# Kernel tuning notes

Measured on AMD Instinct MI355X. Metric: run time of the kernel, lower is better.

## Reference

```python
import jax, jax.numpy as jnp
import numpy as np

N_NODES = 8192
D = 384
N_EDGES = 262144
N_REL = 4
N_LAYERS = 2
BATCH = 64


def setup_inputs() -> dict:
    key = jax.random.key(0)
    ks = jax.random.split(key, 8)
    x = jax.random.normal(ks[0], (N_NODES, D), jnp.float32)
    edge_index = jax.random.randint(ks[1], (2, N_EDGES), 0, N_NODES, dtype=jnp.int32)
    edge_type = jax.random.randint(ks[2], (N_EDGES,), 0, N_REL, dtype=jnp.int32)
    s = 1.0 / np.sqrt(D)
    W_rel = jax.random.uniform(ks[3], (N_LAYERS, N_REL, D, D), jnp.float32, -s, s)
    b_rel = jnp.zeros((N_LAYERS, N_REL, D), jnp.float32)
    norm_const = jnp.ones((N_LAYERS, N_REL), jnp.float32)
    W_msg = jax.random.uniform(ks[4], (N_LAYERS, D, D), jnp.float32, -s, s)
    b_msg = jnp.zeros((N_LAYERS, D), jnp.float32)
    W_self = jax.random.uniform(ks[5], (N_LAYERS, D, D), jnp.float32, -s, s)
    b_self = jnp.zeros((N_LAYERS, D), jnp.float32)
    bn_gamma = jnp.ones((D,), jnp.float32)
    bn_beta = jnp.zeros((D,), jnp.float32)
    return {"x": x, "edge_index": edge_index, "edge_type": edge_type,
            "bn_gamma": bn_gamma, "bn_beta": bn_beta,
            "W_rel": W_rel, "b_rel": b_rel, "norm_const": norm_const,
            "W_msg": W_msg, "b_msg": b_msg, "W_self": W_self, "b_self": b_self,
            "batch_size": BATCH}


def _seg_sum(v, idx, n):
    return jax.ops.segment_sum(v, idx, num_segments=n)


def _forward(x, bn_gamma, bn_beta, W_rel, b_rel, norm_const, W_msg, b_msg,
             W_self, b_self, edge_index, edge_type, batch_size):
    n = x.shape[0]
    # BatchNorm1d (training-mode batch stats) on the utterance embeddings
    mu = x.mean(axis=0)
    var = x.var(axis=0)
    h = bn_gamma * (x - mu) * jax.lax.rsqrt(var + 1e-5) + bn_beta
    src, dst = edge_index[0], edge_index[1]  # PyG: row=source(j), col=target(i)
    # pairwise cosine similarity, gathered only at the edges actually used:
    # edge_weights[dst, src] = <h_dst, h_src> / (|h_dst||h_src|)
    xn = h / jnp.linalg.norm(h, axis=1, keepdims=True)
    w_e = jnp.sum(xn[dst] * xn[src], axis=-1)  # [E]
    ones_e = jnp.ones(src.shape[0], jnp.float32)
    n_layers, n_rel = W_rel.shape[0], W_rel.shape[1]
    for l in range(n_layers):
        # RelationAwareMP: per-relation linear + weighted scatter-mean, summed
        out = jnp.zeros((n, W_rel.shape[2]), h.dtype)
        for r in range(n_rel):
            mask = (edge_type == r).astype(h.dtype)  # [E]
            xr = h @ W_rel[l, r].T + b_rel[l, r]  # [N, D]
            coef = mask * w_e / norm_const[l, r]  # [E]
            s = _seg_sum(coef[:, None] * xr[src], dst, n)
            c = _seg_sum(mask, dst, n)
            out = out + s / jnp.maximum(c, 1.0)[:, None]
        rel_out = jax.nn.relu(out)
        # MP: relu(mean_j lin(x_j) + self_lin(x)), then residual
        mj = rel_out @ W_msg[l].T + b_msg[l]
        s = _seg_sum(mj[src], dst, n)
        c = _seg_sum(ones_e, dst, n)
        aggr = s / jnp.maximum(c, 1.0)[:, None]
        h = jax.nn.relu(aggr + rel_out @ W_self[l].T + b_self[l]) + h
    return h.reshape(batch_size, -1, h.shape[-1]).mean(axis=1)


def reference(x, edge_index, edge_type, bn_gamma, bn_beta, W_rel, b_rel,
              norm_const, W_msg, b_msg, W_self, b_self, batch_size):
    return _forward(x, bn_gamma, bn_beta, W_rel, b_rel, norm_const,
                    W_msg, b_msg, W_self, b_self,
                    edge_index, edge_type, batch_size)
```

## Files before the change

kernel.cpp:

```cpp
#include <hip/hip_runtime.h>
#include <hip/hip_bf16.h>

#define NN 8192
#define DD 384
#define NE 262144
#define NR 4
#define NL 2
#define NB 64

typedef __attribute__((ext_vector_type(8))) short bf16x8;
typedef __attribute__((ext_vector_type(4))) float f32x4;

__device__ __forceinline__ unsigned short f2bf(float f) {
  unsigned u = __float_as_uint(f);
  unsigned r = (u + 0x7fffu + ((u >> 16) & 1u)) >> 16;
  return (unsigned short)r;
}
__device__ __forceinline__ unsigned pack_bf2(float lo, float hi) {
  return (unsigned)f2bf(lo) | ((unsigned)f2bf(hi) << 16);
}
__device__ __forceinline__ float bflo(unsigned u) { return __uint_as_float(u << 16); }
__device__ __forceinline__ float bfhi(unsigned u) { return __uint_as_float(u & 0xffff0000u); }
__device__ __forceinline__ void gl_lds16(const void* g, void* l) {
  __builtin_amdgcn_global_load_lds(
      (const __attribute__((address_space(1))) unsigned int*)g,
      (__attribute__((address_space(3))) unsigned int*)l, 16, 0, 0);
}
__device__ __forceinline__ float dot8(uint4 a, uint4 b) {
  return bflo(a.x) * bflo(b.x) + bfhi(a.x) * bfhi(b.x) +
         bflo(a.y) * bflo(b.y) + bfhi(a.y) * bfhi(b.y) +
         bflo(a.z) * bflo(b.z) + bfhi(a.z) * bfhi(b.z) +
         bflo(a.w) * bflo(b.w) + bfhi(a.w) * bfhi(b.w);
}

__global__ void k_zero(uint4* __restrict__ p, int n4) {
  int i = blockIdx.x * 256 + threadIdx.x;
  if (i < n4) p[i] = make_uint4(0, 0, 0, 0);
}

__global__ void k_colstats(const float* __restrict__ x, float* __restrict__ musum,
                           float* __restrict__ msqsum) {
  int c = threadIdx.x;
  int r0 = blockIdx.x * 32;
  float s = 0.f, s2 = 0.f;
  for (int r = 0; r < 32; ++r) {
    float v = x[(size_t)(r0 + r) * DD + c];
    s += v; s2 += v * v;
  }
  atomicAdd(&musum[c], s);
  atomicAdd(&msqsum[c], s2);
}

__global__ void k_bn(const float* __restrict__ x, const float* __restrict__ gamma,
                     const float* __restrict__ beta, const float* __restrict__ musum,
                     const float* __restrict__ msqsum, float* __restrict__ h,
                     short* __restrict__ h_bf, float* __restrict__ ninv) {
  int n = blockIdx.x;
  int t = threadIdx.x;
  float ss = 0.f;
#pragma unroll
  for (int i = 0; i < 6; ++i) {
    int c = t + i * 64;
    float m = musum[c] * (1.f / NN);
    float var = msqsum[c] * (1.f / NN) - m * m;
    float v = gamma[c] * (x[(size_t)n * DD + c] - m) * rsqrtf(var + 1e-5f) + beta[c];
    h[(size_t)n * DD + c] = v;
    h_bf[(size_t)n * DD + c] = (short)f2bf(v);
    ss += v * v;
  }
#pragma unroll
  for (int m = 32; m; m >>= 1) ss += __shfl_xor(ss, m, 64);
  if (t == 0) ninv[n] = rsqrtf(ss);
}

__global__ void k_counts(const int* __restrict__ ei, const int* __restrict__ et,
                         int* __restrict__ c_rel) {
  int e = blockIdx.x * blockDim.x + threadIdx.x;
  if (e >= NE) return;
  int dst = ei[NE + e];
  atomicAdd(&c_rel[dst * NR + et[e]], 1);
}

__global__ void k_scan(const int* __restrict__ c_rel, int* __restrict__ rp2,
                       int* __restrict__ cursor) {
  __shared__ int part[1024];
  int t = threadIdx.x;
  int base = t * 32;
  int v[32]; int s = 0;
#pragma unroll
  for (int i = 0; i < 32; ++i) { v[i] = c_rel[base + i]; s += v[i]; }
  part[t] = s;
  __syncthreads();
  for (int off = 1; off < 1024; off <<= 1) {
    int add = (t >= off) ? part[t - off] : 0;
    __syncthreads();
    part[t] += add;
    __syncthreads();
  }
  int run = (t == 0) ? 0 : part[t - 1];
  if (t == 0) rp2[0] = 0;
#pragma unroll
  for (int i = 0; i < 32; ++i) {
    cursor[base + i] = run;
    run += v[i];
    rp2[base + i + 1] = run;
  }
}

__global__ void k_fill(const int* __restrict__ ei, const int* __restrict__ et,
                       int* __restrict__ cursor, int* __restrict__ meta) {
  int e = blockIdx.x * blockDim.x + threadIdx.x;
  if (e >= NE) return;
  int src = ei[e], dst = ei[NE + e];
  int pos = atomicAdd(&cursor[dst * NR + et[e]], 1);
  meta[pos] = src;
}

__global__ void k_we2(const short* __restrict__ hb, const float* __restrict__ ninv,
                      const int* __restrict__ rp2, const int* __restrict__ meta,
                      float* __restrict__ wsort) {
  int n = blockIdx.x;
  int g = threadIdx.x >> 4, sl = threadIdx.x & 15;
  int beg = rp2[n * 4], end = rp2[n * 4 + 4];
  if (beg == end) return;
  const uint4* hd = (const uint4*)(hb + (size_t)n * DD);
  uint4 b0 = hd[sl], b1 = hd[16 + sl], b2 = hd[32 + sl];
  float nd = ninv[n];
  for (int s = beg + g; s < end; s += 16) {
    int src = meta[s];
    const uint4* hs = (const uint4*)(hb + (size_t)src * DD);
    float acc = dot8(hs[sl], b0) + dot8(hs[16 + sl], b1) + dot8(hs[32 + sl], b2);
#pragma unroll
    for (int m = 8; m; m >>= 1) acc += __shfl_xor(acc, m, 64);
    if (sl == 0) wsort[s] = acc * ninv[src] * nd;
  }
}

__global__ void k_aggrel(const short* __restrict__ hb, const int* __restrict__ rp2,
                         const int* __restrict__ meta, const float* __restrict__ wsort,
                         const float* __restrict__ nc, short* __restrict__ Agg,
                         float* __restrict__ SC, int layer) {
  int n = blockIdx.x;
  int t = threadIdx.x;
  int r = t / 96;
  int i = t - r * 96;
  int beg = rp2[n * 4 + r], end = rp2[n * 4 + r + 1];
  float a0 = 0, a1 = 0, a2 = 0, a3 = 0, s = 0;
  int e = beg;
  for (; e + 3 < end; e += 4) {
    int s0 = meta[e], s1 = meta[e + 1], s2 = meta[e + 2], s3 = meta[e + 3];
    float w0 = wsort[e], w1 = wsort[e + 1], w2 = wsort[e + 2], w3 = wsort[e + 3];
    uint2 u0 = ((const uint2*)(hb + (size_t)s0 * DD))[i];
    uint2 u1 = ((const uint2*)(hb + (size_t)s1 * DD))[i];
    uint2 u2 = ((const uint2*)(hb + (size_t)s2 * DD))[i];
    uint2 u3 = ((const uint2*)(hb + (size_t)s3 * DD))[i];
    a0 += w0 * bflo(u0.x) + w1 * bflo(u1.x) + w2 * bflo(u2.x) + w3 * bflo(u3.x);
    a1 += w0 * bfhi(u0.x) + w1 * bfhi(u1.x) + w2 * bfhi(u2.x) + w3 * bfhi(u3.x);
    a2 += w0 * bflo(u0.y) + w1 * bflo(u1.y) + w2 * bflo(u2.y) + w3 * bflo(u3.y);
    a3 += w0 * bfhi(u0.y) + w1 * bfhi(u1.y) + w2 * bfhi(u2.y) + w3 * bfhi(u3.y);
    s += w0 + w1 + w2 + w3;
  }
  for (; e < end; ++e) {
    int s0 = meta[e];
    float w0 = wsort[e];
    uint2 u0 = ((const uint2*)(hb + (size_t)s0 * DD))[i];
    a0 += w0 * bflo(u0.x); a1 += w0 * bfhi(u0.x);
    a2 += w0 * bflo(u0.y); a3 += w0 * bfhi(u0.y);
    s += w0;
  }
  int c = end - beg;
  float f = 1.f / (nc[layer * 4 + r] * (float)(c > 1 ? c : 1));
  uint2 o;
  o.x = pack_bf2(a0 * f, a1 * f);
  o.y = pack_bf2(a2 * f, a3 * f);
  ((uint2*)(Agg + (size_t)n * 1536 + r * 384))[i] = o;
  if (i == 0) SC[n * 4 + r] = s * f;
}

__global__ void k_aggmp(short* __restrict__ B1, const int* __restrict__ rp2,
                        const int* __restrict__ meta) {
  __shared__ float red[3][96][4];
  int n = blockIdx.x;
  int t = threadIdx.x;
  int g = t / 96, i = t - g * 96;
  int beg = rp2[n * 4], end = rp2[n * 4 + 4];
  float a0 = 0, a1 = 0, a2 = 0, a3 = 0;
  int e = beg + g;
  for (; e + 12 < end; e += 16) {
    int s0 = meta[e], s1 = meta[e + 4], s2 = meta[e + 8], s3 = meta[e + 12];
    uint2 u0 = ((const uint2*)(B1 + (size_t)s0 * 768 + 384))[i];
    uint2 u1 = ((const uint2*)(B1 + (size_t)s1 * 768 + 384))[i];
    uint2 u2 = ((const uint2*)(B1 + (size_t)s2 * 768 + 384))[i];
    uint2 u3 = ((const uint2*)(B1 + (size_t)s3 * 768 + 384))[i];
    a0 += bflo(u0.x) + bflo(u1.x) + bflo(u2.x) + bflo(u3.x);
    a1 += bfhi(u0.x) + bfhi(u1.x) + bfhi(u2.x) + bfhi(u3.x);
    a2 += bflo(u0.y) + bflo(u1.y) + bflo(u2.y) + bflo(u3.y);
    a3 += bfhi(u0.y) + bfhi(u1.y) + bfhi(u2.y) + bfhi(u3.y);
  }
  for (; e < end; e += 4) {
    int s0 = meta[e];
    uint2 u = ((const uint2*)(B1 + (size_t)s0 * 768 + 384))[i];
    a0 += bflo(u.x); a1 += bfhi(u.x);
    a2 += bflo(u.y); a3 += bfhi(u.y);
  }
  if (g) {
    red[g - 1][i][0] = a0; red[g - 1][i][1] = a1;
    red[g - 1][i][2] = a2; red[g - 1][i][3] = a3;
  }
  __syncthreads();
  if (g == 0) {
#pragma unroll
    for (int k = 0; k < 3; ++k) {
      a0 += red[k][i][0]; a1 += red[k][i][1];
      a2 += red[k][i][2]; a3 += red[k][i][3];
    }
    float inv = (end > beg) ? 1.f / (float)(end - beg) : 0.f;
    uint2 o;
    o.x = pack_bf2(a0 * inv, a1 * inv);
    o.y = pack_bf2(a2 * inv, a3 * inv);
    ((uint2*)(B1 + (size_t)n * 768))[i] = o;
  }
}

__global__ void k_packall(const float* __restrict__ W_rel, const float* __restrict__ W_msg,
                          const float* __restrict__ W_self, short* __restrict__ Wcat,
                          short* __restrict__ Wcat2) {
  const int T1 = NL * 384 * 1536;
  const int T2 = NL * 384 * 768;
  int idx = blockIdx.x * blockDim.x + threadIdx.x;
  if (idx < T1) {
    int l = idx / (384 * 1536);
    int rem = idx - l * 384 * 1536;
    int i = rem / 1536, kk = rem - i * 1536;
    int r = kk / 384, k = kk - r * 384;
    Wcat[idx] = (short)f2bf(W_rel[(((size_t)(l * NR + r) * DD) + i) * DD + k]);
  } else if (idx < T1 + T2) {
    int j = idx - T1;
    int l = j / (384 * 768);
    int rem = j - l * 384 * 768;
    int i = rem / 768, kk = rem - i * 768;
    float v = (kk < 384) ? W_msg[((size_t)l * DD + i) * DD + kk]
                         : W_self[((size_t)l * DD + i) * DD + kk - 384];
    Wcat2[j] = (short)f2bf(v);
  }
}

template <int MODE>
__global__ __launch_bounds__(256) void k_gemm_mfma(
    const short* __restrict__ A, int K, const short* __restrict__ Bp,
    const float* __restrict__ SC, const float* __restrict__ brel_l,
    const float* __restrict__ bmsg_l, const float* __restrict__ bself_l,
    const int* __restrict__ rp2, float* __restrict__ h,
    short* __restrict__ h_bf, short* __restrict__ Cout) {
  __shared__ short As[2][64 * 64];
  __shared__ short Bs[2][64 * 64];
  int tid = threadIdx.x;
  int lane = tid & 63;
  int w = tid >> 6;
  int wr = w >> 1, wc = w & 1;
  int bid = blockIdx.x;
  int wg = ((bid & 7) * 96) + (bid >> 3);
  int bm = wg / 6, bn = wg - bm * 6;

  int r0 = (w << 3) + (lane >> 3);
  int qg = (lane & 7) ^ (r0 & 7);
  const short* Ag0 = A + (size_t)(bm * 64 + r0) * K + qg * 8;
  const short* Ag1 = A + (size_t)(bm * 64 + r0 + 32) * K + qg * 8;
  const short* Bg0 = Bp + (size_t)(bn * 64 + r0) * K + qg * 8;
  const short* Bg1 = Bp + (size_t)(bn * 64 + r0 + 32) * K + qg * 8;

  auto stage = [&](int bi, int k0) {
    gl_lds16(Ag0 + k0, &As[bi][w * 512]);
    gl_lds16(Ag1 + k0, &As[bi][2048 + w * 512]);
    gl_lds16(Bg0 + k0, &Bs[bi][w * 512]);
    gl_lds16(Bg1 + k0, &Bs[bi][2048 + w * 512]);
  };

  f32x4 acc[2][2] = {};
  int fr = lane & 15, fq = lane >> 4;
  int nt = K >> 6;
  stage(0, 0);
  __syncthreads();
  for (int t = 0; t < nt; ++t) {
    if (t + 1 < nt) stage((t + 1) & 1, (t + 1) << 6);
    const short* Ab = As[t & 1];
    const short* Bb = Bs[t & 1];
#pragma unroll
    for (int kk = 0; kk < 2; ++kk) {
      bf16x8 a[2], b[2];
#pragma unroll
      for (int i = 0; i < 2; ++i) {
        int r = wr * 32 + i * 16 + fr;
        int qs = (kk * 4 + fq) ^ (r & 7);
        a[i] = *(const bf16x8*)&Ab[r * 64 + qs * 8];
      }
#pragma unroll
      for (int j = 0; j < 2; ++j) {
        int r = wc * 32 + j * 16 + fr;
        int qs = (kk * 4 + fq) ^ (r & 7);
        b[j] = *(const bf16x8*)&Bb[r * 64 + qs * 8];
      }
#pragma unroll
      for (int i = 0; i < 2; ++i)
#pragma unroll
        for (int j = 0; j < 2; ++j)
          acc[i][j] = __builtin_amdgcn_mfma_f32_16x16x32_bf16(a[i], b[j], acc[i][j], 0, 0, 0);
    }
    __syncthreads();
  }

  int cr = (lane >> 4) * 4;
  int cc = lane & 15;
#pragma unroll
  for (int i = 0; i < 2; ++i) {
#pragma unroll
    for (int jj = 0; jj < 4; ++jj) {
      int row = bm * 64 + wr * 32 + i * 16 + cr + jj;
      if (MODE == 0) {
        float4 sc = *(const float4*)&SC[row * 4];
#pragma unroll
        for (int j = 0; j < 2; ++j) {
          int col = bn * 64 + wc * 32 + j * 16 + cc;
          float v = acc[i][j][jj] + sc.x * brel_l[col] + sc.y * brel_l[384 + col] +
                    sc.z * brel_l[768 + col] + sc.w * brel_l[1152 + col];
          Cout[(size_t)row * 768 + 384 + col] = (short)f2bf(fmaxf(v, 0.f));
        }
      } else {
        float bmul = (rp2[(row + 1) * 4] > rp2[row * 4]) ? 1.f : 0.f;
#pragma unroll
        for (int j = 0; j < 2; ++j) {
          int col = bn * 64 + wc * 32 + j * 16 + cc;
          float v = acc[i][j][jj] + bmul * bmsg_l[col] + bself_l[col];
          float o = fmaxf(v, 0.f) + h[(size_t)row * DD + col];
          h[(size_t)row * DD + col] = o;
          h_bf[(size_t)row * DD + col] = (short)f2bf(o);
        }
      }
    }
  }
}

__global__ void k_out(const float* __restrict__ h, float* __restrict__ out) {
  int b = blockIdx.x;
  int c = threadIdx.x;
  float s = 0.f;
  for (int j = 0; j < 128; ++j) s += h[(size_t)(b * 128 + j) * DD + c];
  out[b * DD + c] = s * (1.f / 128.f);
}

extern "C" void kernel_launch(void* const* d_in, const int* in_sizes, int n_in,
                              void* d_out, int out_size, void* d_ws, size_t ws_size,
                              hipStream_t stream) {
  const float* x      = (const float*)d_in[0];
  const int*   ei     = (const int*)d_in[1];
  const int*   et     = (const int*)d_in[2];
  const float* gamma  = (const float*)d_in[3];
  const float* beta   = (const float*)d_in[4];
  const float* W_rel  = (const float*)d_in[5];
  const float* b_rel  = (const float*)d_in[6];
  const float* nc     = (const float*)d_in[7];
  const float* W_msg  = (const float*)d_in[8];
  const float* b_msg  = (const float*)d_in[9];
  const float* W_self = (const float*)d_in[10];
  const float* b_self = (const float*)d_in[11];
  float* out = (float*)d_out;

  char* ws = (char*)d_ws;
  size_t off = 0;
  auto alloc = [&](size_t bytes) -> void* {
    void* p = ws + off;
    off = (off + bytes + 255) & ~(size_t)255;
    return p;
  };
  float* h      = (float*)alloc((size_t)NN * DD * 4);
  short* h_bf   = (short*)alloc((size_t)NN * DD * 2);
  short* Agg    = (short*)alloc((size_t)NN * 1536 * 2);
  short* B1     = (short*)alloc((size_t)NN * 768 * 2);
  short* Wcat   = (short*)alloc((size_t)NL * 384 * 1536 * 2);
  short* Wcat2  = (short*)alloc((size_t)NL * 384 * 768 * 2);
  float* SC     = (float*)alloc((size_t)NN * 4 * 4);
  int*   meta   = (int*)alloc((size_t)NE * 4);
  float* wsort  = (float*)alloc((size_t)NE * 4);
  int*   rp2    = (int*)alloc((size_t)(NN * 4 + 1) * 4);
  int*   cursor = (int*)alloc((size_t)NN * 4 * 4);
  float* ninv   = (float*)alloc((size_t)NN * 4);
  char*  zb     = (char*)alloc(134144);
  float* musum  = (float*)(zb);
  float* msqsum = (float*)(zb + 1536);
  int*   c_rel  = (int*)(zb + 3072);

  k_zero<<<(134144 / 16 + 255) / 256, 256, 0, stream>>>((uint4*)zb, 134144 / 16);
  k_colstats<<<256, 384, 0, stream>>>(x, musum, msqsum);
  k_bn<<<NN, 64, 0, stream>>>(x, gamma, beta, musum, msqsum, h, h_bf, ninv);
  k_counts<<<NE / 256, 256, 0, stream>>>(ei, et, c_rel);
  k_scan<<<1, 1024, 0, stream>>>(c_rel, rp2, cursor);
  k_fill<<<NE / 256, 256, 0, stream>>>(ei, et, cursor, meta);
  k_we2<<<NN, 256, 0, stream>>>(h_bf, ninv, rp2, meta, wsort);
  k_packall<<<(NL * 384 * 1536 + NL * 384 * 768 + 255) / 256, 256, 0, stream>>>(
      W_rel, W_msg, W_self, Wcat, Wcat2);

  for (int l = 0; l < NL; ++l) {
    k_aggrel<<<NN, 384, 0, stream>>>(h_bf, rp2, meta, wsort, nc, Agg, SC, l);
    k_gemm_mfma<0><<<768, 256, 0, stream>>>(
        Agg, 1536, Wcat + (size_t)l * 384 * 1536, SC, b_rel + l * NR * DD,
        nullptr, nullptr, nullptr, nullptr, nullptr, B1);
    k_aggmp<<<NN, 384, 0, stream>>>(B1, rp2, meta);
    k_gemm_mfma<1><<<768, 256, 0, stream>>>(
        B1, 768, Wcat2 + (size_t)l * 384 * 768, nullptr, nullptr,
        b_msg + l * DD, b_self + l * DD, rp2, h, h_bf, nullptr);
  }
  k_out<<<64, 384, 0, stream>>>(h, out);
}
```

Before: 304.4 us.

## Enlarge GEMM tiles to 128x128 with single-buffered K=32 staging

Switches the MFMA GEMM from 64x64 output tiles with a double-buffered K=64 LDS pipeline to 128x128 tiles, where each wave computes a 4x4 grid of 16x16 fragments and K advances in single-buffered steps of 32. The grid drops from 768 to 192 blocks. The larger tile is meant to improve operand reuse and cut global and LDS traffic per MFMA. In exchange it removes the XOR swizzle and the load/compute overlap, adds two barriers per K step, and leaves fewer blocks than the 256 CUs, so part of the GPU sits idle.

```diff
diff --git a/kernel.cpp b/kernel.cpp
--- a/kernel.cpp
+++ b/kernel.cpp
@@ -252,75 +252,61 @@
     const float* __restrict__ bmsg_l, const float* __restrict__ bself_l,
     const int* __restrict__ rp2, float* __restrict__ h,
     short* __restrict__ h_bf, short* __restrict__ Cout) {
-  __shared__ short As[2][64 * 64];
-  __shared__ short Bs[2][64 * 64];
+  __shared__ short As[128 * 32];
+  __shared__ short Bs[128 * 32];
   int tid = threadIdx.x;
   int lane = tid & 63;
   int w = tid >> 6;
   int wr = w >> 1, wc = w & 1;
   int bid = blockIdx.x;
-  int wg = ((bid & 7) * 96) + (bid >> 3);
-  int bm = wg / 6, bn = wg - bm * 6;
-
-  int r0 = (w << 3) + (lane >> 3);
-  int qg = (lane & 7) ^ (r0 & 7);
-  const short* Ag0 = A + (size_t)(bm * 64 + r0) * K + qg * 8;
-  const short* Ag1 = A + (size_t)(bm * 64 + r0 + 32) * K + qg * 8;
-  const short* Bg0 = Bp + (size_t)(bn * 64 + r0) * K + qg * 8;
-  const short* Bg1 = Bp + (size_t)(bn * 64 + r0 + 32) * K + qg * 8;
-
-  auto stage = [&](int bi, int k0) {
-    gl_lds16(Ag0 + k0, &As[bi][w * 512]);
-    gl_lds16(Ag1 + k0, &As[bi][2048 + w * 512]);
-    gl_lds16(Bg0 + k0, &Bs[bi][w * 512]);
-    gl_lds16(Bg1 + k0, &Bs[bi][2048 + w * 512]);
-  };
-
-  f32x4 acc[2][2] = {};
-  int fr = lane & 15, fq = lane >> 4;
-  int nt = K >> 6;
-  stage(0, 0);
-  __syncthreads();
-  for (int t = 0; t < nt; ++t) {
-    if (t + 1 < nt) stage((t + 1) & 1, (t + 1) << 6);
-    const short* Ab = As[t & 1];
-    const short* Bb = Bs[t & 1];
-#pragma unroll
-    for (int kk = 0; kk < 2; ++kk) {
-      bf16x8 a[2], b[2];
-#pragma unroll
-      for (int i = 0; i < 2; ++i) {
-        int r = wr * 32 + i * 16 + fr;
-        int qs = (kk * 4 + fq) ^ (r & 7);
-        a[i] = *(const bf16x8*)&Ab[r * 64 + qs * 8];
-      }
-#pragma unroll
-      for (int j = 0; j < 2; ++j) {
-        int r = wc * 32 + j * 16 + fr;
-        int qs = (kk * 4 + fq) ^ (r & 7);
-        b[j] = *(const bf16x8*)&Bb[r * 64 + qs * 8];
-      }
-#pragma unroll
-      for (int i = 0; i < 2; ++i)
-#pragma unroll
-        for (int j = 0; j < 2; ++j)
-          acc[i][j] = __builtin_amdgcn_mfma_f32_16x16x32_bf16(a[i], b[j], acc[i][j], 0, 0, 0);
-    }
+  int wg = ((bid & 7) * 24) + (bid >> 3);
+  int bm = wg / 3, bn = wg - bm * 3;
+
+  int r0 = tid >> 2, c0 = (tid & 3) * 8;
+  const short* Ag0 = A + (size_t)(bm * 128 + r0) * K + c0;
+  const short* Ag1 = A + (size_t)(bm * 128 + r0 + 64) * K + c0;
+  const short* Bg0 = Bp + (size_t)(bn * 128 + r0) * K + c0;
+  const short* Bg1 = Bp + (size_t)(bn * 128 + r0 + 64) * K + c0;
+  short* Asl0 = As + w * 512;
+  short* Asl1 = As + 2048 + w * 512;
+  short* Bsl0 = Bs + w * 512;
+  short* Bsl1 = Bs + 2048 + w * 512;
+
+  f32x4 acc[4][4] = {};
+  int fr = lane & 15, fk = (lane >> 4) * 8;
+  for (int k0 = 0; k0 < K; k0 += 32) {
     __syncthreads();
+    gl_lds16(Ag0 + k0, Asl0);
+    gl_lds16(Ag1 + k0, Asl1);
+    gl_lds16(Bg0 + k0, Bsl0);
+    gl_lds16(Bg1 + k0, Bsl1);
+    __syncthreads();
+    bf16x8 a[4], b[4];
+#pragma unroll
+    for (int i = 0; i < 4; ++i)
+      a[i] = *(const bf16x8*)&As[(wr * 64 + i * 16 + fr) * 32 + fk];
+#pragma unroll
+    for (int j = 0; j < 4; ++j)
+      b[j] = *(const bf16x8*)&Bs[(wc * 64 + j * 16 + fr) * 32 + fk];
+#pragma unroll
+    for (int i = 0; i < 4; ++i)
+#pragma unroll
+      for (int j = 0; j < 4; ++j)
+        acc[i][j] = __builtin_amdgcn_mfma_f32_16x16x32_bf16(a[i], b[j], acc[i][j], 0, 0, 0);
   }
 
   int cr = (lane >> 4) * 4;
   int cc = lane & 15;
 #pragma unroll
-  for (int i = 0; i < 2; ++i) {
+  for (int i = 0; i < 4; ++i) {
 #pragma unroll
     for (int jj = 0; jj < 4; ++jj) {
-      int row = bm * 64 + wr * 32 + i * 16 + cr + jj;
+      int row = bm * 128 + wr * 64 + i * 16 + cr + jj;
       if (MODE == 0) {
         float4 sc = *(const float4*)&SC[row * 4];
 #pragma unroll
-        for (int j = 0; j < 2; ++j) {
-          int col = bn * 64 + wc * 32 + j * 16 + cc;
+        for (int j = 0; j < 4; ++j) {
+          int col = bn * 128 + wc * 64 + j * 16 + cc;
           float v = acc[i][j][jj] + sc.x * brel_l[col] + sc.y * brel_l[384 + col] +
                     sc.z * brel_l[768 + col] + sc.w * brel_l[1152 + col];
           Cout[(size_t)row * 768 + 384 + col] = (short)f2bf(fmaxf(v, 0.f));
@@ -328,8 +314,8 @@
       } else {
         float bmul = (rp2[(row + 1) * 4] > rp2[row * 4]) ? 1.f : 0.f;
 #pragma unroll
-        for (int j = 0; j < 2; ++j) {
-          int col = bn * 64 + wc * 32 + j * 16 + cc;
+        for (int j = 0; j < 4; ++j) {
+          int col = bn * 128 + wc * 64 + j * 16 + cc;
           float v = acc[i][j][jj] + bmul * bmsg_l[col] + bself_l[col];
           float o = fmaxf(v, 0.f) + h[(size_t)row * DD + col];
           h[(size_t)row * DD + col] = o;
@@ -401,11 +387,11 @@
 
   for (int l = 0; l < NL; ++l) {
     k_aggrel<<<NN, 384, 0, stream>>>(h_bf, rp2, meta, wsort, nc, Agg, SC, l);
-    k_gemm_mfma<0><<<768, 256, 0, stream>>>(
+    k_gemm_mfma<0><<<192, 256, 0, stream>>>(
         Agg, 1536, Wcat + (size_t)l * 384 * 1536, SC, b_rel + l * NR * DD,
         nullptr, nullptr, nullptr, nullptr, nullptr, B1);
     k_aggmp<<<NN, 384, 0, stream>>>(B1, rp2, meta);
-    k_gemm_mfma<1><<<768, 256, 0, stream>>>(
+    k_gemm_mfma<1><<<192, 256, 0, stream>>>(
         B1, 768, Wcat2 + (size_t)l * 384 * 768, nullptr, nullptr,
         b_msg + l * DD, b_self + l * DD, rp2, h, h_bf, nullptr);
   }
```

New measurement: 395.7 us. 1.3x slower.
